# Kernel tuning notes

Measured on AMD Instinct MI355X. Metric: run time of the kernel, lower is better.

The kernel has to match this reference:

```python
import jax, jax.numpy as jnp
import numpy as np

D_MODEL, D_Q, D_K, D_V, N = 1024, 128, 128, 128, 8192

def setup_inputs() -> dict:
    key = jax.random.key(0)
    ks = jax.random.split(key, 7)
    s = 1.0 / np.sqrt(D_MODEL)
    return {
        "x": jax.random.normal(ks[0], (N, D_MODEL), dtype=jnp.float32),
        "Wq": jax.random.uniform(ks[1], (D_MODEL, D_Q), jnp.float32, -s, s),
        "bq": jax.random.uniform(ks[2], (D_Q,), jnp.float32, -s, s),
        "Wk": jax.random.uniform(ks[3], (D_MODEL, D_K), jnp.float32, -s, s),
        "bk": jax.random.uniform(ks[4], (D_K,), jnp.float32, -s, s),
        "Wv": jax.random.uniform(ks[5], (D_MODEL, D_V), jnp.float32, -s, s),
        "bv": jax.random.uniform(ks[6], (D_V,), jnp.float32, -s, s),
    }

def reference(x, Wq, bq, Wk, bk, Wv, bv):
    q = x @ Wq + bq          # [N, d_q]
    k = x @ Wk + bk          # [N, d_k]
    v = x @ Wv + bv          # [N, d_v]
    scale = jnp.sqrt(jnp.asarray(q.shape[-1], q.dtype))
    scores = (q @ k.T) / scale          # [N, N]
    attn = jax.nn.softmax(scores, axis=1)  # matches nn.Softmax(dim=1) on 2D
    return attn @ v                     # [N, d_v]
```

## Files before the change

### kernel.cpp

```cpp
#include <hip/hip_runtime.h>


typedef __attribute__((ext_vector_type(8))) short bf16x8;
typedef __attribute__((ext_vector_type(4))) float f32x4;

#define NTOK 8192
#define DMODEL 1024
#define DH 128
#define NSPLIT 8
#define CPS 16

__device__ __forceinline__ unsigned short f2bf(float f) {
  unsigned int u = __builtin_bit_cast(unsigned int, f);
  u += 0x7fffu + ((u >> 16) & 1u);
  return (unsigned short)(u >> 16);
}

__device__ __forceinline__ unsigned int pack2bf(float a, float b) {
  return (unsigned int)f2bf(a) | ((unsigned int)f2bf(b) << 16);
}

__device__ __forceinline__ void gl2lds16(const void* gp, void* lp) {
  const __attribute__((address_space(1))) unsigned int* g =
      (const __attribute__((address_space(1))) unsigned int*)gp;
  __attribute__((address_space(3))) unsigned int* l =
      (__attribute__((address_space(3))) unsigned int*)lp;
  __builtin_amdgcn_global_load_lds(g, l, 16, 0, 0);
}

__global__ __launch_bounds__(256) void k_build_wt(const float* __restrict__ Wq,
                                                  const float* __restrict__ Wk,
                                                  const float* __restrict__ Wv,
                                                  unsigned short* __restrict__ wt) {
  __shared__ unsigned short tile[32 * 130];
  int k0 = blockIdx.x * 32;
  int p = blockIdx.y;
  int t = threadIdx.x;
  const float* W = (p == 0) ? Wq : ((p == 1) ? Wk : Wv);
  float vscale = (p == 2) ? 0.0625f : 1.0f;
#pragma unroll
  for (int i = 0; i < 16; i++) {
    int e = i * 256 + t;
    int n = e & 127, kk = e >> 7;
    tile[kk * 130 + n] = f2bf(W[(size_t)(k0 + kk) * DH + n] * vscale);
  }
  __syncthreads();
#pragma unroll
  for (int i = 0; i < 16; i++) {
    int e = i * 256 + t;
    int kk = e & 31, n = e >> 5;
    wt[(size_t)(p * DH + n) * DMODEL + k0 + kk] = tile[kk * 130 + n];
  }
}

__global__ __launch_bounds__(256, 2) void k_qkv(const float* __restrict__ x,
                                                const unsigned short* __restrict__ wt,
                                                const float* __restrict__ bq,
                                                const float* __restrict__ bk,
                                                const float* __restrict__ bv,
                                                unsigned short* __restrict__ qs,
                                                unsigned short* __restrict__ kkv,
                                                unsigned short* __restrict__ vt) {
  __shared__ float xt[2][64 * 64];
  __shared__ unsigned short wtt[2][128 * 64];
  int mt = blockIdx.x, p = blockIdx.y;
  int tid = threadIdx.x;
  int w = tid >> 6, lane = tid & 63, l16 = lane & 15, g = lane >> 4;

#define STAGE_QKV(buf, k0)                                                     \
  {                                                                            \
    _Pragma("unroll") for (int r = 0; r < 4; r++) {                            \
      int seg = r * 4 + w;                                                     \
      int xr = seg * 4 + (lane >> 4);                                          \
      int xlc = ((lane & 15) ^ (xr & 15)) & 15;                                \
      gl2lds16(&x[(size_t)(mt * 64 + xr) * DMODEL + (k0) + xlc * 4],           \
               &xt[buf][seg * 256]);                                           \
      int wc = seg * 8 + (lane >> 3);                                          \
      int wlc = ((lane & 7) ^ (wc & 7)) & 7;                                   \
      gl2lds16(&wt[(size_t)(p * DH + wc) * DMODEL + (k0) + wlc * 8],           \
               &wtt[buf][seg * 512]);                                          \
    }                                                                          \
  }

  f32x4 zero = {0.f, 0.f, 0.f, 0.f};
  f32x4 acc[8];
#pragma unroll
  for (int i = 0; i < 8; i++) acc[i] = zero;

  STAGE_QKV(0, 0);
  int arow = w * 16 + l16;
  for (int kt2 = 0; kt2 < 16; kt2++) {
    int b = kt2 & 1;
    __syncthreads();
    if (kt2 < 15) STAGE_QKV(b ^ 1, (kt2 + 1) * 64);

    bf16x8 a[2];
#pragma unroll
    for (int half = 0; half < 2; half++) {
      int lc0 = half * 8 + g * 2;
      const f32x4 u0 = *(const f32x4*)&xt[b][arow * 64 + ((lc0 ^ l16) & 15) * 4];
      const f32x4 u1 = *(const f32x4*)&xt[b][arow * 64 + (((lc0 + 1) ^ l16) & 15) * 4];
      union { unsigned int u[4]; bf16x8 v; } pk;
      pk.u[0] = pack2bf(u0[0], u0[1]);
      pk.u[1] = pack2bf(u0[2], u0[3]);
      pk.u[2] = pack2bf(u1[0], u1[1]);
      pk.u[3] = pack2bf(u1[2], u1[3]);
      a[half] = pk.v;
    }
#pragma unroll
    for (int nt = 0; nt < 8; nt++) {
      int col = nt * 16 + l16;
#pragma unroll
      for (int half = 0; half < 2; half++) {
        int lc = half * 4 + g;
        bf16x8 bf = *(const bf16x8*)&wtt[b][col * 64 + ((lc ^ (col & 7)) & 7) * 8];
        acc[nt] = __builtin_amdgcn_mfma_f32_16x16x32_bf16(a[half], bf, acc[nt], 0, 0, 0);
      }
    }
  }
#undef STAGE_QKV

  const float* bias = (p == 0) ? bq : ((p == 1) ? bk : bv);
  float mult = (p == 0) ? (0.08838834764831845f * 1.44269504088896340f) : 1.0f;
  if (p < 2) {
    unsigned short* outp = (p == 0) ? qs : kkv;
#pragma unroll
    for (int nt = 0; nt < 8; nt++) {
      int col = nt * 16 + l16;
      float bsv = bias[col];
#pragma unroll
      for (int r = 0; r < 4; r++) {
        int row = mt * 64 + w * 16 + g * 4 + r;
        outp[(size_t)row * DH + col] = f2bf((acc[nt][r] + bsv) * mult);
      }
    }
  } else {
#pragma unroll
    for (int nt = 0; nt < 8; nt++) {
      int col = nt * 16 + l16;
      float bsv = bias[col] * 0.0625f;
      int row0 = mt * 64 + w * 16 + g * 4;
      uint2 uv;
      uv.x = pack2bf(acc[nt][0] + bsv, acc[nt][1] + bsv);
      uv.y = pack2bf(acc[nt][2] + bsv, acc[nt][3] + bsv);
      *(uint2*)(&vt[(size_t)col * NTOK + row0]) = uv;
    }
  }
}

__global__ __launch_bounds__(256, 2) void k_flash(const unsigned short* __restrict__ qs,
                                                  const unsigned short* __restrict__ kkv,
                                                  const unsigned short* __restrict__ vt,
                                                  _Float16* __restrict__ opart,
                                                  float* __restrict__ lpart) {
  __shared__ unsigned short kt[2][64 * 128];
  __shared__ unsigned short vtl[2][128 * 64];
  __shared__ unsigned short pscr[4 * 2 * 1024];
  int sp = blockIdx.x, qt = blockIdx.y;
  int tid = threadIdx.x;
  int w = tid >> 6, lane = tid & 63, l16 = lane & 15, g = lane >> 4;
  int swz2 = (l16 & 7) ^ ((l16 >> 3) << 1);

  bf16x8 qf[2][4];
  int qbase = qt * 128 + w * 32;
#pragma unroll
  for (int q2 = 0; q2 < 2; q2++)
#pragma unroll
    for (int f = 0; f < 4; f++)
      qf[q2][f] = *(const bf16x8*)(&qs[(size_t)(qbase + q2 * 16 + l16) * DH + f * 32 + g * 8]);

  int pcK[4], pcV[2], pcP[2];
#pragma unroll
  for (int f = 0; f < 4; f++) {
    int lc = f * 4 + g;
    pcK[f] = (lc & 8) | ((lc ^ l16) & 7);
  }
#pragma unroll
  for (int kb = 0; kb < 2; kb++) {
    int lc = kb * 4 + g;
    pcV[kb] = (lc ^ l16) & 7;
    pcP[kb] = (lc ^ swz2) & 7;
  }

#define STAGE_FLASH(buf, chunk)                                                 \
  {                                                                             \
    int key0 = (chunk) * 64;                                                    \
    _Pragma("unroll") for (int ii = 0; ii < 4; ii++) {                          \
      int i = w * 4 + ii;                                                       \
      int krow = 4 * i + (lane >> 4);                                           \
      int klc = ((lane & 15) & 8) | (((lane & 15) ^ krow) & 7);                 \
      gl2lds16(&kkv[(size_t)(key0 + krow) * DH + klc * 8], &kt[buf][i * 512]);  \
      int vrow = 8 * i + (lane >> 3);                                           \
      int vlc = ((lane & 7) ^ vrow) & 7;                                        \
      gl2lds16(&vt[(size_t)vrow * NTOK + key0 + vlc * 8], &vtl[buf][i * 512]);  \
    }                                                                           \
  }

  f32x4 zero = {0.f, 0.f, 0.f, 0.f};
  f32x4 o[2][8];
#pragma unroll
  for (int q2 = 0; q2 < 2; q2++)
#pragma unroll
    for (int dt = 0; dt < 8; dt++) o[q2][dt] = zero;
  float l[2] = {0.f, 0.f};

  int c0 = sp * CPS;
  STAGE_FLASH(0, c0);

  for (int it = 0; it < CPS; it++) {
    int b = it & 1;
    __syncthreads();
    if (it + 1 < CPS) STAGE_FLASH(b ^ 1, c0 + it + 1);

    f32x4 s[2][4];
#pragma unroll
    for (int q2 = 0; q2 < 2; q2++)
#pragma unroll
      for (int mt = 0; mt < 4; mt++) s[q2][mt] = zero;
#pragma unroll
    for (int mt = 0; mt < 4; mt++) {
      bf16x8 kf[4];
#pragma unroll
      for (int f = 0; f < 4; f++)
        kf[f] = *(const bf16x8*)(&kt[b][(mt * 16 + l16) * 128 + pcK[f] * 8]);
#pragma unroll
      for (int f = 0; f < 4; f++) {
        s[0][mt] = __builtin_amdgcn_mfma_f32_16x16x32_bf16(kf[f], qf[0][f], s[0][mt], 0, 0, 0);
        s[1][mt] = __builtin_amdgcn_mfma_f32_16x16x32_bf16(kf[f], qf[1][f], s[1][mt], 0, 0, 0);
      }
    }

#pragma unroll
    for (int q2 = 0; q2 < 2; q2++) {
      unsigned short* pw = &pscr[(w * 2 + q2) * 1024];
      float ssum = 0.f;
#pragma unroll
      for (int mt = 0; mt < 4; mt++) {
        float p0 = __builtin_amdgcn_exp2f(s[q2][mt][0]);
        float p1 = __builtin_amdgcn_exp2f(s[q2][mt][1]);
        float p2 = __builtin_amdgcn_exp2f(s[q2][mt][2]);
        float p3 = __builtin_amdgcn_exp2f(s[q2][mt][3]);
        ssum += (p0 + p1) + (p2 + p3);
        uint2 uv;
        uv.x = pack2bf(p0, p1);
        uv.y = pack2bf(p2, p3);
        int ch = ((mt * 2 + (g >> 1)) ^ swz2) & 7;
        *(uint2*)(&pw[l16 * 64 + ch * 8 + (g & 1) * 4]) = uv;
      }
      l[q2] += ssum;
    }

    bf16x8 pb[2][2];
#pragma unroll
    for (int q2 = 0; q2 < 2; q2++)
#pragma unroll
      for (int kb = 0; kb < 2; kb++)
        pb[q2][kb] = *(const bf16x8*)(&pscr[(w * 2 + q2) * 1024 + l16 * 64 + pcP[kb] * 8]);

#pragma unroll
    for (int dt = 0; dt < 8; dt++)
#pragma unroll
      for (int kb = 0; kb < 2; kb++) {
        bf16x8 vf = *(const bf16x8*)(&vtl[b][(dt * 16 + l16) * 64 + pcV[kb] * 8]);
        o[0][dt] = __builtin_amdgcn_mfma_f32_16x16x32_bf16(vf, pb[0][kb], o[0][dt], 0, 0, 0);
        o[1][dt] = __builtin_amdgcn_mfma_f32_16x16x32_bf16(vf, pb[1][kb], o[1][dt], 0, 0, 0);
      }
  }
#undef STAGE_FLASH

#pragma unroll
  for (int q2 = 0; q2 < 2; q2++) {
    l[q2] += __shfl_xor(l[q2], 16);
    l[q2] += __shfl_xor(l[q2], 32);
    int qrow = qbase + q2 * 16 + l16;
    size_t obase = ((size_t)sp * NTOK + qrow) * DH;
#pragma unroll
    for (int dt = 0; dt < 8; dt++) {
      union { _Float16 h[4]; uint2 u; } pk;
      pk.h[0] = (_Float16)o[q2][dt][0];
      pk.h[1] = (_Float16)o[q2][dt][1];
      pk.h[2] = (_Float16)o[q2][dt][2];
      pk.h[3] = (_Float16)o[q2][dt][3];
      *(uint2*)(&opart[obase + dt * 16 + g * 4]) = pk.u;
    }
    if (g == 0) lpart[sp * NTOK + qrow] = l[q2];
  }
}

__global__ __launch_bounds__(256) void k_merge(const _Float16* __restrict__ opart,
                                               const float* __restrict__ lpart,
                                               float* __restrict__ out) {
  int gid = blockIdx.x * 256 + threadIdx.x;
  int row = gid >> 6, cp = gid & 63;
  float den = 0.f, n0 = 0.f, n1 = 0.f;
#pragma unroll
  for (int s = 0; s < NSPLIT; s++) {
    den += lpart[s * NTOK + row];
    union { unsigned int u; _Float16 h[2]; } v;
    v.u = *(const unsigned int*)&opart[((size_t)s * NTOK + row) * DH + cp * 2];
    n0 += (float)v.h[0];
    n1 += (float)v.h[1];
  }
  float inv = 16.0f / den;
  *(float2*)&out[(size_t)row * DH + cp * 2] = make_float2(n0 * inv, n1 * inv);
}

extern "C" void kernel_launch(void* const* d_in, const int* in_sizes, int n_in,
                              void* d_out, int out_size, void* d_ws, size_t ws_size,
                              hipStream_t stream) {
  const float* x  = (const float*)d_in[0];
  const float* Wq = (const float*)d_in[1];
  const float* bq = (const float*)d_in[2];
  const float* Wk = (const float*)d_in[3];
  const float* bk = (const float*)d_in[4];
  const float* Wv = (const float*)d_in[5];
  const float* bv = (const float*)d_in[6];
  float* out = (float*)d_out;

  char* ws = (char*)d_ws;
  _Float16*       opart = (_Float16*)(ws);
  unsigned short* wt  = (unsigned short*)(ws + 16777216);
  unsigned short* qsb = (unsigned short*)(ws + 17563648);
  unsigned short* kkb = (unsigned short*)(ws + 19660800);
  unsigned short* vtb = (unsigned short*)(ws + 21757952);
  float* lpart = (float*)(ws + 23855104);

  k_build_wt<<<dim3(32, 3), 256, 0, stream>>>(Wq, Wk, Wv, wt);
  k_qkv<<<dim3(128, 3), 256, 0, stream>>>(x, wt, bq, bk, bv, qsb, kkb, vtb);
  k_flash<<<dim3(NSPLIT, 64), 256, 0, stream>>>(qsb, kkb, vtb, opart, lpart);
  k_merge<<<2048, 256, 0, stream>>>(opart, lpart, out);
}
```

Baseline: 150.4 us.

## Pre-convert x to bf16 in a prep kernel and feed QKV GEMM bf16 tiles

Adds a prep pass that converts x from fp32 to bf16 into workspace, fused with the weight transpose into one launch. The QKV projection then stages bf16 x tiles directly through LDS, with no per-iteration fp32-to-bf16 packing. The grid is swapped so the three projections of one row tile launch adjacently, which should improve L2 reuse of x. This removes redundant conversions (x was converted three times, once per projection) and halves QKV x read traffic and LDS footprint. The cost is an extra full write and read of a bf16 copy of x (16 MB), and launch_bounds occupancy hint 2 was dropped.

```diff
diff --git a/kernel.cpp b/kernel.cpp
--- a/kernel.cpp
+++ b/kernel.cpp
@@ -28,58 +28,76 @@
   __builtin_amdgcn_global_load_lds(g, l, 16, 0, 0);
 }
 
-__global__ __launch_bounds__(256) void k_build_wt(const float* __restrict__ Wq,
-                                                  const float* __restrict__ Wk,
-                                                  const float* __restrict__ Wv,
-                                                  unsigned short* __restrict__ wt) {
+__global__ __launch_bounds__(256) void k_prep(const float* __restrict__ x,
+                                              const float* __restrict__ Wq,
+                                              const float* __restrict__ Wk,
+                                              const float* __restrict__ Wv,
+                                              unsigned short* __restrict__ xb,
+                                              unsigned short* __restrict__ wt) {
   __shared__ unsigned short tile[32 * 130];
-  int k0 = blockIdx.x * 32;
-  int p = blockIdx.y;
+  int bid = blockIdx.x;
   int t = threadIdx.x;
-  const float* W = (p == 0) ? Wq : ((p == 1) ? Wk : Wv);
-  float vscale = (p == 2) ? 0.0625f : 1.0f;
-#pragma unroll
-  for (int i = 0; i < 16; i++) {
-    int e = i * 256 + t;
-    int n = e & 127, kk = e >> 7;
-    tile[kk * 130 + n] = f2bf(W[(size_t)(k0 + kk) * DH + n] * vscale);
-  }
-  __syncthreads();
-#pragma unroll
-  for (int i = 0; i < 16; i++) {
-    int e = i * 256 + t;
-    int kk = e & 31, n = e >> 5;
-    wt[(size_t)(p * DH + n) * DMODEL + k0 + kk] = tile[kk * 130 + n];
-  }
-}
-
-__global__ __launch_bounds__(256, 2) void k_qkv(const float* __restrict__ x,
-                                                const unsigned short* __restrict__ wt,
-                                                const float* __restrict__ bq,
-                                                const float* __restrict__ bk,
-                                                const float* __restrict__ bv,
-                                                unsigned short* __restrict__ qs,
-                                                unsigned short* __restrict__ kkv,
-                                                unsigned short* __restrict__ vt) {
-  __shared__ float xt[2][64 * 64];
+  if (bid < 4096) {
+    int gid = bid * 256 + t;
+    const float4* src = (const float4*)x;
+    float4 a = src[2 * gid];
+    float4 b = src[2 * gid + 1];
+    union { unsigned short s[8]; uint4 v; } o;
+    o.s[0] = f2bf(a.x); o.s[1] = f2bf(a.y); o.s[2] = f2bf(a.z); o.s[3] = f2bf(a.w);
+    o.s[4] = f2bf(b.x); o.s[5] = f2bf(b.y); o.s[6] = f2bf(b.z); o.s[7] = f2bf(b.w);
+    ((uint4*)xb)[gid] = o.v;
+  } else {
+    int b2 = bid - 4096;
+    int p = b2 >> 5;
+    int k0 = (b2 & 31) * 32;
+    const float* W = (p == 0) ? Wq : ((p == 1) ? Wk : Wv);
+    float vscale = (p == 2) ? 0.0625f : 1.0f;
+#pragma unroll
+    for (int i = 0; i < 16; i++) {
+      int e = i * 256 + t;
+      int n = e & 127, kk = e >> 7;
+      tile[kk * 130 + n] = f2bf(W[(size_t)(k0 + kk) * DH + n] * vscale);
+    }
+    __syncthreads();
+#pragma unroll
+    for (int i = 0; i < 16; i++) {
+      int e = i * 256 + t;
+      int kk = e & 31, n = e >> 5;
+      wt[(size_t)(p * DH + n) * DMODEL + k0 + kk] = tile[kk * 130 + n];
+    }
+  }
+}
+
+__global__ __launch_bounds__(256) void k_qkv(const unsigned short* __restrict__ xb,
+                                             const unsigned short* __restrict__ wt,
+                                             const float* __restrict__ bq,
+                                             const float* __restrict__ bk,
+                                             const float* __restrict__ bv,
+                                             unsigned short* __restrict__ qs,
+                                             unsigned short* __restrict__ kkv,
+                                             unsigned short* __restrict__ vt) {
+  __shared__ unsigned short xt[2][64 * 64];
   __shared__ unsigned short wtt[2][128 * 64];
-  int mt = blockIdx.x, p = blockIdx.y;
+  int p = blockIdx.x, mt = blockIdx.y;
   int tid = threadIdx.x;
   int w = tid >> 6, lane = tid & 63, l16 = lane & 15, g = lane >> 4;
 
-#define STAGE_QKV(buf, k0)                                                     \
-  {                                                                            \
-    _Pragma("unroll") for (int r = 0; r < 4; r++) {                            \
-      int seg = r * 4 + w;                                                     \
-      int xr = seg * 4 + (lane >> 4);                                          \
-      int xlc = ((lane & 15) ^ (xr & 15)) & 15;                                \
-      gl2lds16(&x[(size_t)(mt * 64 + xr) * DMODEL + (k0) + xlc * 4],           \
-               &xt[buf][seg * 256]);                                           \
-      int wc = seg * 8 + (lane >> 3);                                          \
-      int wlc = ((lane & 7) ^ (wc & 7)) & 7;                                   \
-      gl2lds16(&wt[(size_t)(p * DH + wc) * DMODEL + (k0) + wlc * 8],           \
-               &wtt[buf][seg * 512]);                                          \
-    }                                                                          \
+#define STAGE_Q(buf, k0)                                                     \
+  {                                                                          \
+    _Pragma("unroll") for (int ii = 0; ii < 2; ii++) {                       \
+      int i = w * 2 + ii;                                                    \
+      int xrow = i * 8 + (lane >> 3);                                        \
+      int xpc = (lane & 7) ^ (xrow & 7);                                     \
+      gl2lds16(&xb[(size_t)(mt * 64 + xrow) * DMODEL + (k0) + xpc * 8],      \
+               &xt[buf][i * 512]);                                           \
+    }                                                                        \
+    _Pragma("unroll") for (int ii = 0; ii < 4; ii++) {                       \
+      int i = w * 4 + ii;                                                    \
+      int wr = i * 8 + (lane >> 3);                                          \
+      int wpc = (lane & 7) ^ (wr & 7);                                       \
+      gl2lds16(&wt[(size_t)(p * DH + wr) * DMODEL + (k0) + wpc * 8],         \
+               &wtt[buf][i * 512]);                                          \
+    }                                                                        \
   }
 
   f32x4 zero = {0.f, 0.f, 0.f, 0.f};
@@ -87,38 +105,27 @@
 #pragma unroll
   for (int i = 0; i < 8; i++) acc[i] = zero;
 
-  STAGE_QKV(0, 0);
-  int arow = w * 16 + l16;
+  STAGE_Q(0, 0);
+  int arow = w * 16 + l16, r7 = l16 & 7;
+
   for (int kt2 = 0; kt2 < 16; kt2++) {
     int b = kt2 & 1;
     __syncthreads();
-    if (kt2 < 15) STAGE_QKV(b ^ 1, (kt2 + 1) * 64);
-
-    bf16x8 a[2];
-#pragma unroll
-    for (int half = 0; half < 2; half++) {
-      int lc0 = half * 8 + g * 2;
-      const f32x4 u0 = *(const f32x4*)&xt[b][arow * 64 + ((lc0 ^ l16) & 15) * 4];
-      const f32x4 u1 = *(const f32x4*)&xt[b][arow * 64 + (((lc0 + 1) ^ l16) & 15) * 4];
-      union { unsigned int u[4]; bf16x8 v; } pk;
-      pk.u[0] = pack2bf(u0[0], u0[1]);
-      pk.u[1] = pack2bf(u0[2], u0[3]);
-      pk.u[2] = pack2bf(u1[0], u1[1]);
-      pk.u[3] = pack2bf(u1[2], u1[3]);
-      a[half] = pk.v;
-    }
+    if (kt2 < 15) STAGE_Q(b ^ 1, (kt2 + 1) * 64);
+
+    bf16x8 a0 = *(const bf16x8*)&xt[b][arow * 64 + ((g ^ r7) & 7) * 8];
+    bf16x8 a1 = *(const bf16x8*)&xt[b][arow * 64 + (((4 + g) ^ r7) & 7) * 8];
 #pragma unroll
     for (int nt = 0; nt < 8; nt++) {
       int col = nt * 16 + l16;
-#pragma unroll
-      for (int half = 0; half < 2; half++) {
-        int lc = half * 4 + g;
-        bf16x8 bf = *(const bf16x8*)&wtt[b][col * 64 + ((lc ^ (col & 7)) & 7) * 8];
-        acc[nt] = __builtin_amdgcn_mfma_f32_16x16x32_bf16(a[half], bf, acc[nt], 0, 0, 0);
-      }
-    }
-  }
-#undef STAGE_QKV
+      int c7 = col & 7;
+      bf16x8 b0 = *(const bf16x8*)&wtt[b][col * 64 + ((g ^ c7) & 7) * 8];
+      bf16x8 b1 = *(const bf16x8*)&wtt[b][col * 64 + (((4 + g) ^ c7) & 7) * 8];
+      acc[nt] = __builtin_amdgcn_mfma_f32_16x16x32_bf16(a0, b0, acc[nt], 0, 0, 0);
+      acc[nt] = __builtin_amdgcn_mfma_f32_16x16x32_bf16(a1, b1, acc[nt], 0, 0, 0);
+    }
+  }
+#undef STAGE_Q
 
   const float* bias = (p == 0) ? bq : ((p == 1) ? bk : bv);
   float mult = (p == 0) ? (0.08838834764831845f * 1.44269504088896340f) : 1.0f;
@@ -318,6 +325,7 @@
   float* out = (float*)d_out;
 
   char* ws = (char*)d_ws;
+  unsigned short* xb    = (unsigned short*)(ws);
   _Float16*       opart = (_Float16*)(ws);
   unsigned short* wt  = (unsigned short*)(ws + 16777216);
   unsigned short* qsb = (unsigned short*)(ws + 17563648);
@@ -325,8 +333,8 @@
   unsigned short* vtb = (unsigned short*)(ws + 21757952);
   float* lpart = (float*)(ws + 23855104);
 
-  k_build_wt<<<dim3(32, 3), 256, 0, stream>>>(Wq, Wk, Wv, wt);
-  k_qkv<<<dim3(128, 3), 256, 0, stream>>>(x, wt, bq, bk, bv, qsb, kkb, vtb);
+  k_prep<<<4192, 256, 0, stream>>>(x, Wq, Wk, Wv, xb, wt);
+  k_qkv<<<dim3(3, 128), 256, 0, stream>>>(xb, wt, bq, bk, bv, qsb, kkb, vtb);
   k_flash<<<dim3(NSPLIT, 64), 256, 0, stream>>>(qsb, kkb, vtb, opart, lpart);
   k_merge<<<2048, 256, 0, stream>>>(opart, lpart, out);
 }
```

New measurement: 158.2 us. +5.1%, slower.
